# Kernel tuning notes

Hardware: AMD Instinct MI355X
Metric: run time of the kernel (lower is better)

## Reference

```python
import jax, jax.numpy as jnp
import numpy as np

D_MODEL = 512
NUM_HEADS = 8
DEPTH = D_MODEL // NUM_HEADS
MAX_SEQ = 2048
B, L = 4, 1024


def setup_inputs() -> dict:
    key = jax.random.key(0)
    ks = jax.random.split(key, 13)
    s = 0.02
    return {
        "v": jax.random.normal(ks[0], (B, L, D_MODEL), jnp.float32),
        "k": jax.random.normal(ks[1], (B, L, D_MODEL), jnp.float32),
        "q": jax.random.normal(ks[2], (B, L, D_MODEL), jnp.float32),
        "mask": jnp.zeros((1, 1, L, L), jnp.float32),
        "wq_w": jax.random.normal(ks[3], (D_MODEL, D_MODEL), jnp.float32) * s,
        "wq_b": jnp.zeros((D_MODEL,), jnp.float32),
        "wk_w": jax.random.normal(ks[4], (D_MODEL, D_MODEL), jnp.float32) * s,
        "wk_b": jnp.zeros((D_MODEL,), jnp.float32),
        "wv_w": jax.random.normal(ks[5], (D_MODEL, D_MODEL), jnp.float32) * s,
        "wv_b": jnp.zeros((D_MODEL,), jnp.float32),
        "wo_w": jax.random.normal(ks[6], (D_MODEL, D_MODEL), jnp.float32) * s,
        "wo_b": jnp.zeros((D_MODEL,), jnp.float32),
        "pos_emb": jax.random.normal(ks[7], (MAX_SEQ, DEPTH), jnp.float32) * s,
    }


def _split_heads(x, batch):
    # [B, L, d_model] -> [B, H, L, depth]
    return x.reshape(batch, -1, NUM_HEADS, DEPTH).transpose(0, 2, 1, 3)


def reference(v, k, q, mask, wq_w, wq_b, wk_w, wk_b, wv_w, wv_b, wo_w, wo_b, pos_emb):
    batch, l_q, _ = q.shape
    qh = _split_heads(q @ wq_w + wq_b, batch)   # [B,H,Lq,depth]
    kh = _split_heads(k @ wk_w + wk_b, batch)   # [B,H,Lk,depth]
    vh = _split_heads(v @ wv_w + wv_b, batch)   # [B,H,Lk,depth]
    l_k = kh.shape[2]

    # relative position embedding slice: last l_q rows of pos_emb -> [Lq, depth]
    e = pos_emb[max(0, MAX_SEQ - l_q):, :]
    qe = jnp.einsum('nhld,md->nhlm', qh, e)     # [B,H,Lq,Lq]

    # upper-left triangular masking: keep entries with i + j >= Lq - 1
    keep = (jnp.arange(l_q)[:, None] + jnp.arange(l_q)[None, :]) >= (l_q - 1)
    qe = qe * keep.astype(qe.dtype)

    # skew trick: pad left on last dim, reshape [L, L+1]->[L+1, L], drop first row
    padded = jnp.pad(qe, ((0, 0), (0, 0), (0, 0), (1, 0)))
    srel = padded.reshape(batch, NUM_HEADS, l_q + 1, l_q)[:, :, 1:, :]  # [B,H,Lq,Lq]
    if l_k > l_q:
        srel = jnp.pad(srel, ((0, 0), (0, 0), (0, 0), (0, l_k - l_q)))
    elif l_k < l_q:
        srel = srel[..., :l_k]

    scale = 1.0 / jnp.sqrt(jnp.asarray(DEPTH, qh.dtype))
    logits = (jnp.einsum('nhld,nhmd->nhlm', qh, kh) + srel) * scale
    logits = logits + mask * (-1e9)
    attn = jax.nn.softmax(logits, axis=-1)      # [B,H,Lq,Lk]
    ctx = jnp.einsum('nhlm,nhmd->nhld', attn, vh)
    ctx = ctx.transpose(0, 2, 1, 3).reshape(batch, l_q, D_MODEL)
    out = ctx @ wo_w + wo_b
    return out, attn
```

## Files before the change

kernel.cpp:

```cpp
#include <hip/hip_runtime.h>

typedef __attribute__((ext_vector_type(4))) float f32x4;
typedef __attribute__((ext_vector_type(8))) short s16x8;
typedef __attribute__((ext_vector_type(4))) unsigned short u16x4;

__device__ inline unsigned short f2bf(float f) {
  unsigned int u = __builtin_bit_cast(unsigned int, f);
  u += 0x7fff + ((u >> 16) & 1);
  return (unsigned short)(u >> 16);
}
__device__ inline float bf2f(unsigned short u) {
  return __builtin_bit_cast(float, (unsigned int)u << 16);
}

__device__ __forceinline__ void async16(const void* g, void* s) {
  __builtin_amdgcn_global_load_lds(
      (const __attribute__((address_space(1))) unsigned int*)g,
      (__attribute__((address_space(3))) unsigned int*)s, 16, 0, 0);
}

__device__ __forceinline__ void waitv(int n) {
  if (n >= 6)      asm volatile("s_waitcnt vmcnt(6)" ::: "memory");
  else if (n == 4) asm volatile("s_waitcnt vmcnt(4)" ::: "memory");
  else if (n == 2) asm volatile("s_waitcnt vmcnt(2)" ::: "memory");
  else             asm volatile("s_waitcnt vmcnt(0)" ::: "memory");
}

__global__ __launch_bounds__(256) void cast_kernel(
    const float* __restrict__ wq, const float* __restrict__ wk, const float* __restrict__ wv,
    const float* __restrict__ wo, const float* __restrict__ pos,
    unsigned short* __restrict__ wqT, unsigned short* __restrict__ wkT,
    unsigned short* __restrict__ wvT, unsigned short* __restrict__ woT,
    unsigned short* __restrict__ ebf) {
  int seg = blockIdx.y;
  int tid = blockIdx.x * blockDim.x + threadIdx.x;
  int stride = gridDim.x * blockDim.x;
  if (seg < 4) {
    const float* src = seg == 0 ? wq : seg == 1 ? wk : seg == 2 ? wv : wo;
    unsigned short* dst = seg == 0 ? wqT : seg == 1 ? wkT : seg == 2 ? wvT : woT;
    for (int i = tid; i < 512 * 128; i += stride) {
      int n = i >> 7, k0 = (i & 127) * 4;
      u16x4 o = {f2bf(src[(k0 + 0) * 512 + n]), f2bf(src[(k0 + 1) * 512 + n]),
                 f2bf(src[(k0 + 2) * 512 + n]), f2bf(src[(k0 + 3) * 512 + n])};
      *(u16x4*)&dst[n * 512 + k0] = o;
    }
  } else {
    for (int i = tid; i < 1024 * 64 / 4; i += stride) {
      f32x4 x = *(const f32x4*)&pos[1024 * 64 + i * 4];
      u16x4 o = {f2bf(x[0]), f2bf(x[1]), f2bf(x[2]), f2bf(x[3])};
      *(u16x4*)&ebf[i * 4] = o;
    }
  }
}

__global__ __launch_bounds__(256, 2) void proj3_kernel(
    const float* __restrict__ qf, const float* __restrict__ kf,
    const float* __restrict__ vf, const unsigned short* __restrict__ wqT,
    const unsigned short* __restrict__ wkT, const unsigned short* __restrict__ wvT,
    const float* __restrict__ wq_b, const float* __restrict__ wk_b,
    const float* __restrict__ wv_b, unsigned short* __restrict__ qhw,
    unsigned short* __restrict__ khw, unsigned short* __restrict__ vhT) {
  __shared__ unsigned short As[128 * 32];
  __shared__ unsigned short Bs[128 * 32];
  int z = blockIdx.z;
  const float* A = z == 0 ? qf : z == 1 ? kf : vf;
  const unsigned short* Bt = z == 0 ? wqT : z == 1 ? wkT : wvT;
  const float* bias = z == 0 ? wq_b : z == 1 ? wk_b : wv_b;
  unsigned short* outp = z == 0 ? qhw : z == 1 ? khw : vhT;
  int r0 = blockIdx.x * 128, c0 = blockIdx.y * 128;
  int tid = threadIdx.x;
  int lane = tid & 63, w = tid >> 6;
  int wr = w >> 1, wc = w & 1;
  int frow = lane & 15, kg = lane >> 4;
  f32x4 acc[4][4] = {};
  for (int k0 = 0; k0 < 512; k0 += 32) {
#pragma unroll
    for (int j = 0; j < 2; ++j) {
      int t = tid + j * 256;
      int row = t >> 2, col = (t & 3) * 8;
      f32x4 a0 = *(const f32x4*)&A[(size_t)(r0 + row) * 512 + k0 + col];
      f32x4 a1 = *(const f32x4*)&A[(size_t)(r0 + row) * 512 + k0 + col + 4];
      u16x4 p0 = {f2bf(a0[0]), f2bf(a0[1]), f2bf(a0[2]), f2bf(a0[3])};
      u16x4 p1 = {f2bf(a1[0]), f2bf(a1[1]), f2bf(a1[2]), f2bf(a1[3])};
      *(u16x4*)&As[row * 32 + col] = p0;
      *(u16x4*)&As[row * 32 + col + 4] = p1;
      *(s16x8*)&Bs[row * 32 + col] = *(const s16x8*)&Bt[(size_t)(c0 + row) * 512 + k0 + col];
    }
    __syncthreads();
    s16x8 af[4], bfr[4];
#pragma unroll
    for (int mi = 0; mi < 4; ++mi) af[mi] = *(s16x8*)&As[(wr * 64 + mi * 16 + frow) * 32 + kg * 8];
#pragma unroll
    for (int ni = 0; ni < 4; ++ni) bfr[ni] = *(s16x8*)&Bs[(wc * 64 + ni * 16 + frow) * 32 + kg * 8];
#pragma unroll
    for (int mi = 0; mi < 4; ++mi)
#pragma unroll
      for (int ni = 0; ni < 4; ++ni)
        acc[mi][ni] = __builtin_amdgcn_mfma_f32_16x16x32_bf16(af[mi], bfr[ni], acc[mi][ni], 0, 0, 0);
    __syncthreads();
  }
#pragma unroll
  for (int ni = 0; ni < 4; ++ni) {
    int gc = c0 + wc * 64 + ni * 16 + frow;
    float bi = bias[gc];
#pragma unroll
    for (int mi = 0; mi < 4; ++mi) {
#pragma unroll
      for (int reg = 0; reg < 4; ++reg) {
        int gr = r0 + wr * 64 + mi * 16 + kg * 4 + reg;
        float val = acc[mi][ni][reg] + bi;
        if (z != 2) {
          outp[(size_t)((gr >> 10) * 8 + (gc >> 6)) * 65536 +
               (size_t)(gr & 1023) * 64 + (gc & 63)] = f2bf(val);
        } else {
          outp[(size_t)((gr >> 10) * 8 + (gc >> 6)) * 65536 +
               (size_t)(gc & 63) * 1024 + (gr & 1023)] = f2bf(val);
        }
      }
    }
  }
}

__global__ __launch_bounds__(256, 2) void gemm_out_kernel(
    const unsigned short* __restrict__ A, const unsigned short* __restrict__ Bt,
    const float* __restrict__ bias, float* __restrict__ outp) {
  __shared__ unsigned short As[128 * 32];
  __shared__ unsigned short Bs[128 * 32];
  int r0 = blockIdx.x * 128, c0 = blockIdx.y * 128;
  int tid = threadIdx.x;
  int lane = tid & 63, w = tid >> 6;
  int wr = w >> 1, wc = w & 1;
  int frow = lane & 15, kg = lane >> 4;
  f32x4 acc[4][4] = {};
  for (int k0 = 0; k0 < 512; k0 += 32) {
#pragma unroll
    for (int j = 0; j < 2; ++j) {
      int t = tid + j * 256;
      int row = t >> 2, col = (t & 3) * 8;
      *(s16x8*)&As[row * 32 + col] = *(const s16x8*)&A[(size_t)(r0 + row) * 512 + k0 + col];
      *(s16x8*)&Bs[row * 32 + col] = *(const s16x8*)&Bt[(size_t)(c0 + row) * 512 + k0 + col];
    }
    __syncthreads();
    s16x8 af[4], bfr[4];
#pragma unroll
    for (int mi = 0; mi < 4; ++mi) af[mi] = *(s16x8*)&As[(wr * 64 + mi * 16 + frow) * 32 + kg * 8];
#pragma unroll
    for (int ni = 0; ni < 4; ++ni) bfr[ni] = *(s16x8*)&Bs[(wc * 64 + ni * 16 + frow) * 32 + kg * 8];
#pragma unroll
    for (int mi = 0; mi < 4; ++mi)
#pragma unroll
      for (int ni = 0; ni < 4; ++ni)
        acc[mi][ni] = __builtin_amdgcn_mfma_f32_16x16x32_bf16(af[mi], bfr[ni], acc[mi][ni], 0, 0, 0);
    __syncthreads();
  }
#pragma unroll
  for (int ni = 0; ni < 4; ++ni) {
    int gc = c0 + wc * 64 + ni * 16 + frow;
    float bi = bias[gc];
#pragma unroll
    for (int mi = 0; mi < 4; ++mi)
#pragma unroll
      for (int reg = 0; reg < 4; ++reg) {
        int gr = r0 + wr * 64 + mi * 16 + kg * 4 + reg;
        outp[(size_t)gr * 512 + gc] = acc[mi][ni][reg] + bi;
      }
  }
}

__global__ __launch_bounds__(256, 2) void attn_kernel(
    const unsigned short* __restrict__ qh, const unsigned short* __restrict__ kh,
    const unsigned short* __restrict__ vhT, const unsigned short* __restrict__ ebf,
    const float* __restrict__ mask, float* __restrict__ attn_out,
    unsigned short* __restrict__ ctx) {
  __shared__ unsigned short S[16 * 1024];
  __shared__ unsigned short KV[4][4096];
  __shared__ float redmax[4][16], redsum[4][16];
  int fid = blockIdx.x;
  int nh = ((fid & 7) << 2) | ((fid >> 3) & 3);
  int l0 = (fid >> 5) << 4;
  int tid = threadIdx.x;
  int lane = tid & 63, w = tid >> 6;
  int frow = lane & 15, kg = lane >> 4;

  auto sp = [&](int r, int c) -> unsigned short* {
    int byte = (r << 11) + (c << 1);
    byte ^= (r & 7) << 4;
    return (unsigned short*)((char*)S + byte);
  };

  auto stageKE = [&](const unsigned short* srcbase, int buf) {
#pragma unroll
    for (int i = 0; i < 2; ++i) {
      int rl = i * 8 + (lane >> 3);
      int p = lane & 7;
      async16(srcbase + (size_t)(w * 16 + rl) * 64 + p * 8,
              &KV[buf][w * 1024 + i * 512]);
    }
  };
  auto stageV = [&](const unsigned short* vsrc, int c, int buf) {
#pragma unroll
    for (int i = 0; i < 2; ++i) {
      int rl = i * 8 + (lane >> 3);
      int p = lane & 7;
      async16(vsrc + (size_t)(w * 16 + rl) * 1024 + c * 64 + p * 8,
              &KV[buf][w * 1024 + i * 512]);
    }
  };

  const unsigned short* qbase = qh + ((size_t)nh * 1024 + l0 + frow) * 64 + kg * 8;
  s16x8 qf0 = *(const s16x8*)(qbase);
  s16x8 qf1 = *(const s16x8*)(qbase + 32);

  int cmin = 1008 - l0;
  int cstart = cmin >> 6;
#pragma unroll
  for (int i = 0; i < 4; ++i)
    if (cstart + i < 16) stageKE(ebf + (size_t)(cstart + i) * 4096, (cstart + i) & 3);
  for (int c = cstart; c < 16; ++c) {
    int buf = c & 3;
    int rem = 15 - c;
    waitv(2 * (rem > 3 ? 3 : rem));
    __builtin_amdgcn_sched_barrier(0);
    int j0 = c * 64 + w * 16;
    if (j0 + 15 >= cmin) {
      const char* base = (const char*)&KV[buf][0] + w * 2048 + frow * 128;
      s16x8 b0 = *(const s16x8*)(base + (kg << 4));
      s16x8 b1 = *(const s16x8*)(base + ((4 + kg) << 4));
      f32x4 a = {};
      a = __builtin_amdgcn_mfma_f32_16x16x32_bf16(b0, qf0, a, 0, 0, 0);
      a = __builtin_amdgcn_mfma_f32_16x16x32_bf16(b1, qf1, a, 0, 0, 0);
      u16x4 pk = {f2bf(a[0]), f2bf(a[1]), f2bf(a[2]), f2bf(a[3])};
      *(u16x4*)sp(frow, j0 + kg * 4) = pk;
    }
    asm volatile("s_waitcnt lgkmcnt(0)" ::: "memory");
    __builtin_amdgcn_sched_barrier(0);
    if (c + 4 < 16) stageKE(ebf + (size_t)(c + 4) * 4096, buf);
  }
  const unsigned short* kbase = kh + (size_t)nh * 65536;
#pragma unroll
  for (int i = 0; i < 4; ++i) stageKE(kbase + (size_t)i * 4096, i);
  __syncthreads();

  f32x4 lg[16];
#pragma unroll
  for (int c = 0; c < 16; ++c) {
    int buf = c & 3;
    int rem = 15 - c;
    waitv(2 * (rem > 3 ? 3 : rem));
    __builtin_amdgcn_sched_barrier(0);
    const char* base = (const char*)&KV[buf][0] + w * 2048 + frow * 128;
    s16x8 b0 = *(const s16x8*)(base + (kg << 4));
    s16x8 b1 = *(const s16x8*)(base + ((4 + kg) << 4));
    f32x4 a = {};
    a = __builtin_amdgcn_mfma_f32_16x16x32_bf16(b0, qf0, a, 0, 0, 0);
    a = __builtin_amdgcn_mfma_f32_16x16x32_bf16(b1, qf1, a, 0, 0, 0);
    lg[c] = a;
    asm volatile("s_waitcnt lgkmcnt(0)" ::: "memory");
    __builtin_amdgcn_sched_barrier(0);
    if (c + 4 < 16) stageKE(kbase + (size_t)(c + 4) * 4096, buf);
  }

  int lq = l0 + frow;
#pragma unroll
  for (int c = 0; c < 16; ++c) {
    int m0k = c * 64 + w * 16 + kg * 4;
    f32x4 mk = *(const f32x4*)&mask[(size_t)lq * 1024 + m0k];
#pragma unroll
    for (int reg = 0; reg < 4; ++reg) {
      int m = m0k + reg;
      float srel = (m <= lq) ? bf2f(*sp(frow, 1023 + m - lq)) : 0.f;
      lg[c][reg] = (lg[c][reg] + srel) * 0.125f + mk[reg] * -1e9f;
    }
  }

  f32x4 vmax = lg[0];
#pragma unroll
  for (int c = 1; c < 16; ++c) {
#pragma unroll
    for (int reg = 0; reg < 4; ++reg) vmax[reg] = fmaxf(vmax[reg], lg[c][reg]);
  }
  float mx = fmaxf(fmaxf(vmax[0], vmax[1]), fmaxf(vmax[2], vmax[3]));
  mx = fmaxf(mx, __shfl_xor(mx, 16));
  mx = fmaxf(mx, __shfl_xor(mx, 32));
  float s = 0.f;
#pragma unroll
  for (int c = 0; c < 16; ++c) {
#pragma unroll
    for (int reg = 0; reg < 4; ++reg) {
      lg[c][reg] = __expf(lg[c][reg] - mx);
      s += lg[c][reg];
    }
  }
  s += __shfl_xor(s, 16);
  s += __shfl_xor(s, 32);
  if (lane < 16) {
    redmax[w][lane] = mx;
    redsum[w][lane] = s;
  }
  __syncthreads();

  float gmax = fmaxf(fmaxf(redmax[0][frow], redmax[1][frow]),
                     fmaxf(redmax[2][frow], redmax[3][frow]));
  float gsum = redsum[0][frow] * __expf(redmax[0][frow] - gmax) +
               redsum[1][frow] * __expf(redmax[1][frow] - gmax) +
               redsum[2][frow] * __expf(redmax[2][frow] - gmax) +
               redsum[3][frow] * __expf(redmax[3][frow] - gmax);
  float fac = __expf(mx - gmax) / gsum;

  size_t arow = ((size_t)nh * 1024 + lq) * 1024;
#pragma unroll
  for (int c = 0; c < 16; ++c) {
    int m0k = c * 64 + w * 16 + kg * 4;
    f32x4 pn;
#pragma unroll
    for (int reg = 0; reg < 4; ++reg) pn[reg] = lg[c][reg] * fac;
    *(f32x4*)&attn_out[arow + m0k] = pn;
    u16x4 pb = {f2bf(pn[0]), f2bf(pn[1]), f2bf(pn[2]), f2bf(pn[3])};
    *(u16x4*)sp(frow, m0k) = pb;
  }
  const unsigned short* vsrc = vhT + (size_t)nh * 65536;
#pragma unroll
  for (int i = 0; i < 4; ++i) stageV(vsrc, i, i);
  __syncthreads();

  {
    f32x4 acc = {};
#pragma unroll
    for (int c = 0; c < 16; ++c) {
      int buf = c & 3;
      int rem = 15 - c;
      waitv(2 * (rem > 3 ? 3 : rem));
      __builtin_amdgcn_sched_barrier(0);
      const char* vbase = (const char*)&KV[buf][0] + w * 2048 + frow * 128;
#pragma unroll
      for (int ks = 0; ks < 2; ++ks) {
        s16x8 a = *(s16x8*)sp(frow, c * 64 + ks * 32 + kg * 8);
        s16x8 b = *(const s16x8*)(vbase + ((ks * 4 + kg) << 4));
        acc = __builtin_amdgcn_mfma_f32_16x16x32_bf16(a, b, acc, 0, 0, 0);
      }
      asm volatile("s_waitcnt lgkmcnt(0)" ::: "memory");
      __builtin_amdgcn_sched_barrier(0);
      if (c + 4 < 16) stageV(vsrc, c + 4, buf);
    }
    int n = nh >> 3, h = nh & 7;
#pragma unroll
    for (int reg = 0; reg < 4; ++reg) {
      int rr = kg * 4 + reg;
      ctx[((size_t)(n * 1024 + l0 + rr)) * 512 + h * 64 + w * 16 + frow] = f2bf(acc[reg]);
    }
  }
}

extern "C" void kernel_launch(void* const* d_in, const int* in_sizes, int n_in,
                              void* d_out, int out_size, void* d_ws, size_t ws_size,
                              hipStream_t stream) {
  const float* v = (const float*)d_in[0];
  const float* k = (const float*)d_in[1];
  const float* q = (const float*)d_in[2];
  const float* mask = (const float*)d_in[3];
  const float* wq_w = (const float*)d_in[4];
  const float* wq_b = (const float*)d_in[5];
  const float* wk_w = (const float*)d_in[6];
  const float* wk_b = (const float*)d_in[7];
  const float* wv_w = (const float*)d_in[8];
  const float* wv_b = (const float*)d_in[9];
  const float* wo_w = (const float*)d_in[10];
  const float* wo_b = (const float*)d_in[11];
  const float* pos = (const float*)d_in[12];

  float* outp = (float*)d_out;
  float* attn_out = outp + (size_t)4 * 1024 * 512;

  char* ws = (char*)d_ws;
  unsigned short* ctx = (unsigned short*)(ws);
  unsigned short* wqT = (unsigned short*)(ws + ((size_t)12 << 20));
  unsigned short* wkT = (unsigned short*)(ws + ((size_t)12 << 20) + (512 << 10));
  unsigned short* wvT = (unsigned short*)(ws + ((size_t)13 << 20));
  unsigned short* woT = (unsigned short*)(ws + ((size_t)13 << 20) + (512 << 10));
  unsigned short* ebf = (unsigned short*)(ws + ((size_t)14 << 20));
  unsigned short* qhw = (unsigned short*)(ws + ((size_t)16 << 20));
  unsigned short* khw = (unsigned short*)(ws + ((size_t)20 << 20));
  unsigned short* vhT = (unsigned short*)(ws + ((size_t)24 << 20));

  cast_kernel<<<dim3(256, 5), 256, 0, stream>>>(wq_w, wk_w, wv_w, wo_w, pos,
                                                wqT, wkT, wvT, woT, ebf);
  proj3_kernel<<<dim3(32, 4, 3), 256, 0, stream>>>(q, k, v, wqT, wkT, wvT,
                                                   wq_b, wk_b, wv_b, qhw, khw, vhT);
  attn_kernel<<<2048, 256, 0, stream>>>(qhw, khw, vhT, ebf, mask, attn_out, ctx);
  gemm_out_kernel<<<dim3(32, 4), 256, 0, stream>>>(ctx, woT, wo_b, outp);
}
```

Baseline: 128.0 us.

## Enlarge attention block to 64 query rows sharing staged K/E/V tiles

Restructures the attention kernel so each 1024-thread block handles 64 query rows, with four row groups sharing each K, positional-embedding and V tile loaded into LDS. Staging goes to double buffering issued by half the warps with block barriers, and an XOR swizzle is added to the staged tiles to avoid bank conflicts. The aim is to cut redundant global/LDS traffic per query row. The cost is a 128KB score buffer that limits occupancy, heavier register pressure per thread, and more block-wide barriers.

```diff
diff --git a/kernel.cpp b/kernel.cpp
--- a/kernel.cpp
+++ b/kernel.cpp
@@ -17,13 +17,6 @@
   __builtin_amdgcn_global_load_lds(
       (const __attribute__((address_space(1))) unsigned int*)g,
       (__attribute__((address_space(3))) unsigned int*)s, 16, 0, 0);
-}
-
-__device__ __forceinline__ void waitv(int n) {
-  if (n >= 6)      asm volatile("s_waitcnt vmcnt(6)" ::: "memory");
-  else if (n == 4) asm volatile("s_waitcnt vmcnt(4)" ::: "memory");
-  else if (n == 2) asm volatile("s_waitcnt vmcnt(2)" ::: "memory");
-  else             asm volatile("s_waitcnt vmcnt(0)" ::: "memory");
 }
 
 __global__ __launch_bounds__(256) void cast_kernel(
@@ -167,20 +160,23 @@
   }
 }
 
-__global__ __launch_bounds__(256, 2) void attn_kernel(
+__global__ __launch_bounds__(1024, 4) void attn_kernel(
     const unsigned short* __restrict__ qh, const unsigned short* __restrict__ kh,
     const unsigned short* __restrict__ vhT, const unsigned short* __restrict__ ebf,
     const float* __restrict__ mask, float* __restrict__ attn_out,
     unsigned short* __restrict__ ctx) {
-  __shared__ unsigned short S[16 * 1024];
-  __shared__ unsigned short KV[4][4096];
-  __shared__ float redmax[4][16], redsum[4][16];
+  __shared__ unsigned short S[64 * 1024];
+  __shared__ unsigned short KV[2][4096];
+  __shared__ float redmax[16][16], redsum[16][16];
   int fid = blockIdx.x;
   int nh = ((fid & 7) << 2) | ((fid >> 3) & 3);
-  int l0 = (fid >> 5) << 4;
+  int ltile = fid >> 5;
+  int l0 = ltile << 6;
   int tid = threadIdx.x;
   int lane = tid & 63, w = tid >> 6;
+  int rg = w >> 2, ms = w & 3;
   int frow = lane & 15, kg = lane >> 4;
+  int qrow = rg * 16 + frow;
 
   auto sp = [&](int r, int c) -> unsigned short* {
     int byte = (r << 11) + (c << 1);
@@ -189,86 +185,92 @@
   };
 
   auto stageKE = [&](const unsigned short* srcbase, int buf) {
-#pragma unroll
-    for (int i = 0; i < 2; ++i) {
-      int rl = i * 8 + (lane >> 3);
+    if (w < 8) {
+      int rl = w * 8 + (lane >> 3);
       int p = lane & 7;
-      async16(srcbase + (size_t)(w * 16 + rl) * 64 + p * 8,
-              &KV[buf][w * 1024 + i * 512]);
+      async16(srcbase + (size_t)rl * 64 + ((p ^ (rl & 7)) * 8), &KV[buf][w * 512]);
     }
   };
   auto stageV = [&](const unsigned short* vsrc, int c, int buf) {
-#pragma unroll
-    for (int i = 0; i < 2; ++i) {
-      int rl = i * 8 + (lane >> 3);
+    if (w < 8) {
+      int dr = w * 8 + (lane >> 3);
       int p = lane & 7;
-      async16(vsrc + (size_t)(w * 16 + rl) * 1024 + c * 64 + p * 8,
-              &KV[buf][w * 1024 + i * 512]);
+      async16(vsrc + (size_t)dr * 1024 + c * 64 + ((p ^ (dr & 7)) * 8),
+              &KV[buf][w * 512]);
     }
   };
-
-  const unsigned short* qbase = qh + ((size_t)nh * 1024 + l0 + frow) * 64 + kg * 8;
+  auto waitv1 = [&]() { if (w < 8) asm volatile("s_waitcnt vmcnt(1)" ::: "memory"); };
+  auto waitv0 = [&]() { if (w < 8) asm volatile("s_waitcnt vmcnt(0)" ::: "memory"); };
+  auto bar = [&]() {
+    __builtin_amdgcn_s_barrier();
+    __builtin_amdgcn_sched_barrier(0);
+  };
+
+  const unsigned short* qbase = qh + ((size_t)nh * 1024 + l0 + qrow) * 64 + kg * 8;
   s16x8 qf0 = *(const s16x8*)(qbase);
   s16x8 qf1 = *(const s16x8*)(qbase + 32);
 
-  int cmin = 1008 - l0;
-  int cstart = cmin >> 6;
-#pragma unroll
-  for (int i = 0; i < 4; ++i)
-    if (cstart + i < 16) stageKE(ebf + (size_t)(cstart + i) * 4096, (cstart + i) & 3);
+  int rx = frow & 7;
+
+  int cmin = 960 - l0;
+  int cstart = 15 - ltile;
+  stageKE(ebf + (size_t)cstart * 4096, cstart & 1);
+  if (cstart + 1 < 16) stageKE(ebf + (size_t)(cstart + 1) * 4096, (cstart + 1) & 1);
   for (int c = cstart; c < 16; ++c) {
-    int buf = c & 3;
-    int rem = 15 - c;
-    waitv(2 * (rem > 3 ? 3 : rem));
-    __builtin_amdgcn_sched_barrier(0);
-    int j0 = c * 64 + w * 16;
+    int buf = c & 1;
+    if (c + 1 < 16) waitv1(); else waitv0();
+    bar();
+    int j0 = c * 64 + ms * 16;
     if (j0 + 15 >= cmin) {
-      const char* base = (const char*)&KV[buf][0] + w * 2048 + frow * 128;
-      s16x8 b0 = *(const s16x8*)(base + (kg << 4));
-      s16x8 b1 = *(const s16x8*)(base + ((4 + kg) << 4));
+      const char* base = (const char*)&KV[buf][0] + (ms * 16 + frow) * 128;
+      s16x8 b0 = *(const s16x8*)(base + ((kg ^ rx) << 4));
+      s16x8 b1 = *(const s16x8*)(base + (((4 + kg) ^ rx) << 4));
       f32x4 a = {};
       a = __builtin_amdgcn_mfma_f32_16x16x32_bf16(b0, qf0, a, 0, 0, 0);
       a = __builtin_amdgcn_mfma_f32_16x16x32_bf16(b1, qf1, a, 0, 0, 0);
       u16x4 pk = {f2bf(a[0]), f2bf(a[1]), f2bf(a[2]), f2bf(a[3])};
-      *(u16x4*)sp(frow, j0 + kg * 4) = pk;
+      *(u16x4*)sp(qrow, j0 + kg * 4) = pk;
     }
     asm volatile("s_waitcnt lgkmcnt(0)" ::: "memory");
-    __builtin_amdgcn_sched_barrier(0);
-    if (c + 4 < 16) stageKE(ebf + (size_t)(c + 4) * 4096, buf);
+    bar();
+    if (c + 2 < 16) stageKE(ebf + (size_t)(c + 2) * 4096, buf);
   }
   const unsigned short* kbase = kh + (size_t)nh * 65536;
-#pragma unroll
-  for (int i = 0; i < 4; ++i) stageKE(kbase + (size_t)i * 4096, i);
+  stageKE(kbase, 0);
+  stageKE(kbase + 4096, 1);
   __syncthreads();
 
   f32x4 lg[16];
 #pragma unroll
   for (int c = 0; c < 16; ++c) {
-    int buf = c & 3;
-    int rem = 15 - c;
-    waitv(2 * (rem > 3 ? 3 : rem));
-    __builtin_amdgcn_sched_barrier(0);
-    const char* base = (const char*)&KV[buf][0] + w * 2048 + frow * 128;
-    s16x8 b0 = *(const s16x8*)(base + (kg << 4));
-    s16x8 b1 = *(const s16x8*)(base + ((4 + kg) << 4));
+    int buf = c & 1;
+    if (c + 1 < 16) waitv1(); else waitv0();
+    bar();
+    const char* base = (const char*)&KV[buf][0] + (ms * 16 + frow) * 128;
+    s16x8 b0 = *(const s16x8*)(base + ((kg ^ rx) << 4));
+    s16x8 b1 = *(const s16x8*)(base + (((4 + kg) ^ rx) << 4));
     f32x4 a = {};
     a = __builtin_amdgcn_mfma_f32_16x16x32_bf16(b0, qf0, a, 0, 0, 0);
     a = __builtin_amdgcn_mfma_f32_16x16x32_bf16(b1, qf1, a, 0, 0, 0);
     lg[c] = a;
     asm volatile("s_waitcnt lgkmcnt(0)" ::: "memory");
-    __builtin_amdgcn_sched_barrier(0);
-    if (c + 4 < 16) stageKE(kbase + (size_t)(c + 4) * 4096, buf);
-  }
-
-  int lq = l0 + frow;
+    bar();
+    if (c + 2 < 16) stageKE(kbase + (size_t)(c + 2) * 4096, buf);
+  }
+
+  const unsigned short* vsrc = vhT + (size_t)nh * 65536;
+  stageV(vsrc, 0, 0);
+  stageV(vsrc, 1, 1);
+
+  int lq = l0 + qrow;
 #pragma unroll
   for (int c = 0; c < 16; ++c) {
-    int m0k = c * 64 + w * 16 + kg * 4;
+    int m0k = c * 64 + ms * 16 + kg * 4;
     f32x4 mk = *(const f32x4*)&mask[(size_t)lq * 1024 + m0k];
 #pragma unroll
     for (int reg = 0; reg < 4; ++reg) {
       int m = m0k + reg;
-      float srel = (m <= lq) ? bf2f(*sp(frow, 1023 + m - lq)) : 0.f;
+      float srel = (m <= lq) ? bf2f(*sp(qrow, 1023 + m - lq)) : 0.f;
       lg[c][reg] = (lg[c][reg] + srel) * 0.125f + mk[reg] * -1e9f;
     }
   }
@@ -299,54 +301,51 @@
   }
   __syncthreads();
 
-  float gmax = fmaxf(fmaxf(redmax[0][frow], redmax[1][frow]),
-                     fmaxf(redmax[2][frow], redmax[3][frow]));
-  float gsum = redsum[0][frow] * __expf(redmax[0][frow] - gmax) +
-               redsum[1][frow] * __expf(redmax[1][frow] - gmax) +
-               redsum[2][frow] * __expf(redmax[2][frow] - gmax) +
-               redsum[3][frow] * __expf(redmax[3][frow] - gmax);
+  float gmax = redmax[rg * 4 + 0][frow];
+#pragma unroll
+  for (int i = 1; i < 4; ++i) gmax = fmaxf(gmax, redmax[rg * 4 + i][frow]);
+  float gsum = 0.f;
+#pragma unroll
+  for (int i = 0; i < 4; ++i)
+    gsum += redsum[rg * 4 + i][frow] * __expf(redmax[rg * 4 + i][frow] - gmax);
   float fac = __expf(mx - gmax) / gsum;
 
   size_t arow = ((size_t)nh * 1024 + lq) * 1024;
 #pragma unroll
   for (int c = 0; c < 16; ++c) {
-    int m0k = c * 64 + w * 16 + kg * 4;
+    int m0k = c * 64 + ms * 16 + kg * 4;
     f32x4 pn;
 #pragma unroll
     for (int reg = 0; reg < 4; ++reg) pn[reg] = lg[c][reg] * fac;
     *(f32x4*)&attn_out[arow + m0k] = pn;
     u16x4 pb = {f2bf(pn[0]), f2bf(pn[1]), f2bf(pn[2]), f2bf(pn[3])};
-    *(u16x4*)sp(frow, m0k) = pb;
-  }
-  const unsigned short* vsrc = vhT + (size_t)nh * 65536;
-#pragma unroll
-  for (int i = 0; i < 4; ++i) stageV(vsrc, i, i);
+    *(u16x4*)sp(qrow, m0k) = pb;
+  }
   __syncthreads();
 
   {
     f32x4 acc = {};
 #pragma unroll
     for (int c = 0; c < 16; ++c) {
-      int buf = c & 3;
-      int rem = 15 - c;
-      waitv(2 * (rem > 3 ? 3 : rem));
-      __builtin_amdgcn_sched_barrier(0);
-      const char* vbase = (const char*)&KV[buf][0] + w * 2048 + frow * 128;
+      int buf = c & 1;
+      if (c + 1 < 16) waitv1(); else waitv0();
+      bar();
+      const char* vbase = (const char*)&KV[buf][0] + (ms * 16 + frow) * 128;
 #pragma unroll
       for (int ks = 0; ks < 2; ++ks) {
-        s16x8 a = *(s16x8*)sp(frow, c * 64 + ks * 32 + kg * 8);
-        s16x8 b = *(const s16x8*)(vbase + ((ks * 4 + kg) << 4));
+        s16x8 a = *(s16x8*)sp(qrow, c * 64 + ks * 32 + kg * 8);
+        s16x8 b = *(const s16x8*)(vbase + (((ks * 4 + kg) ^ rx) << 4));
         acc = __builtin_amdgcn_mfma_f32_16x16x32_bf16(a, b, acc, 0, 0, 0);
       }
       asm volatile("s_waitcnt lgkmcnt(0)" ::: "memory");
-      __builtin_amdgcn_sched_barrier(0);
-      if (c + 4 < 16) stageV(vsrc, c + 4, buf);
+      bar();
+      if (c + 2 < 16) stageV(vsrc, c + 2, buf);
     }
     int n = nh >> 3, h = nh & 7;
 #pragma unroll
     for (int reg = 0; reg < 4; ++reg) {
-      int rr = kg * 4 + reg;
-      ctx[((size_t)(n * 1024 + l0 + rr)) * 512 + h * 64 + w * 16 + frow] = f2bf(acc[reg]);
+      int rr = rg * 16 + kg * 4 + reg;
+      ctx[((size_t)(n * 1024 + l0 + rr)) * 512 + h * 64 + ms * 16 + frow] = f2bf(acc[reg]);
     }
   }
 }
@@ -386,6 +385,6 @@
                                                 wqT, wkT, wvT, woT, ebf);
   proj3_kernel<<<dim3(32, 4, 3), 256, 0, stream>>>(q, k, v, wqT, wkT, wvT,
                                                    wq_b, wk_b, wv_b, qhw, khw, vhT);
-  attn_kernel<<<2048, 256, 0, stream>>>(qhw, khw, vhT, ebf, mask, attn_out, ctx);
+  attn_kernel<<<512, 1024, 0, stream>>>(qhw, khw, vhT, ebf, mask, attn_out, ctx);
   gemm_out_kernel<<<dim3(32, 4), 256, 0, stream>>>(ctx, woT, wo_b, outp);
 }
```

After: 203.2 us. 1.59x slower.
